# Optimization experiments

Hardware: AMD Instinct MI355X
Metric: run time of the kernel (lower is better)

Reference implementation:

```python
import jax, jax.numpy as jnp
import numpy as np
import math

BATCH, D_MODEL, D_STATE, SEQ_L = 8, 256, 64, 2048


def setup_inputs() -> dict:
    key = jax.random.key(0)
    k0, k1, k2, k3 = jax.random.split(key, 4)
    x = jax.random.normal(k0, (BATCH, D_MODEL, SEQ_L), dtype=jnp.float32)
    # A = -exp(A_real) - 1j*A_imag  (S4D-Lin style init: A = -0.5 + i*pi*n)
    A_real = jnp.full((D_MODEL, D_STATE), jnp.log(0.5), dtype=jnp.float32)
    A_imag = -jnp.broadcast_to(math.pi * jnp.arange(D_STATE, dtype=jnp.float32), (D_MODEL, D_STATE))
    # B, C stored as real view of complex: (1, H, N, 2)
    B = jax.random.normal(k1, (1, D_MODEL, D_STATE, 2), dtype=jnp.float32)
    C = jax.random.normal(k2, (1, D_MODEL, D_STATE, 2), dtype=jnp.float32)
    # inv_dt: log-uniform in [log(1e-3), log(1e-1)], shape (H, 1)
    u = jax.random.uniform(k3, (D_MODEL, 1), dtype=jnp.float32)
    inv_dt = u * (math.log(0.1) - math.log(0.001)) + math.log(0.001)
    return {"x": x, "A_real": A_real, "A_imag": A_imag, "B": B, "C": C, "inv_dt": inv_dt}


def reference(x, A_real, A_imag, B, C, inv_dt):
    L = x.shape[-1]
    # --- _get_params ---
    A = -jnp.exp(A_real) - 1j * A_imag            # (H, N) complex poles
    dt = jnp.exp(inv_dt)                           # (H, 1)
    Bc = B[..., 0] + 1j * B[..., 1]                # (1, H, N)
    Cc = C[..., 0] + 1j * C[..., 1]                # (1, H, N)
    # --- compute_kernel ---
    dtA = dt * A                                   # (H, N) = log of discrete-time pole
    Ceff = (Bc * Cc) * (jnp.exp(dtA) - 1.0) / A    # (1, H, N)
    # log-Vandermonde: K = 2*Re sum_n Ceff * exp(dtA)^l  -> (1, H, L)
    ell = jnp.arange(L, dtype=jnp.float32)
    vand = jnp.exp(dtA[:, :, None] * ell)          # (H, N, L) complex
    k = 2.0 * jnp.real(jnp.einsum('chn,hnl->chl', Ceff, vand))  # (1, H, L)
    # --- FFT convolution ---
    n = 2 * L
    k_f = jnp.fft.rfft(k, n=n)                     # (1, H, L+1)
    x_f = jnp.fft.rfft(x, n=n)                     # (B, H, L+1)
    y_f = jnp.einsum('bhl,chl->bchl', x_f, k_f)    # (B, 1, H, L+1)
    y = jnp.fft.irfft(y_f, n=n)[..., :L]           # (B, 1, H, L)
    return jax.nn.relu(y)
```

## Files before the change

### kernel.cpp

```cpp
#include <hip/hip_runtime.h>


#define B_ 8
#define H_ 256
#define N_ 64
#define L_ 2048
#define Q_ 64
#define NC_ 32
#define COLS_ 128
#define PKSTR_ 68
#define PLSTR_ 72

typedef __attribute__((ext_vector_type(8))) short bf16x8;
typedef __attribute__((ext_vector_type(4))) float f32x4;

#define WS_W1R  0
#define WS_W1I  (WS_W1R + 2097152)
#define WS_TL   (WS_W1I + 2097152)
#define WS_W2R  (WS_TL  + 2097152)
#define WS_W2I  (WS_W2R + 2097152)

#if defined(__has_builtin)
#  if __has_builtin(__builtin_amdgcn_cvt_pk_bf16_f32)
#    define HAVE_CVT_PK 1
#  endif
#endif

__device__ __forceinline__ unsigned short bf16_rne(float f) {
    unsigned int u = __float_as_uint(f);
    u += 0x7FFF + ((u >> 16) & 1);
    return (unsigned short)(u >> 16);
}
__device__ __forceinline__ float bf16_to_f(unsigned short h) {
    return __uint_as_float(((unsigned int)h) << 16);
}
__device__ __forceinline__ unsigned int pack_bf16x2(float a, float b) {
#ifdef HAVE_CVT_PK
    typedef __bf16 bf16v2 __attribute__((ext_vector_type(2)));
    bf16v2 p = __builtin_amdgcn_cvt_pk_bf16_f32(a, b);
    return __builtin_bit_cast(unsigned int, p);
#else
    unsigned int ua = __float_as_uint(a);
    ua += 0x7FFF + ((ua >> 16) & 1);
    unsigned int ub = __float_as_uint(b);
    ub += 0x7FFF + ((ub >> 16) & 1);
    return (ua >> 16) | (ub & 0xFFFF0000u);
#endif
}

__global__ __launch_bounds__(64) void s4d_prep(
    const float* __restrict__ A_real, const float* __restrict__ A_imag,
    const float* __restrict__ Bmat, const float* __restrict__ Cmat,
    const float* __restrict__ inv_dt,
    unsigned short* __restrict__ W1sr, unsigned short* __restrict__ W1si,
    unsigned short* __restrict__ TLs,
    unsigned short* __restrict__ W2sr, unsigned short* __restrict__ W2si)
{
    __shared__ float lds[64 * 68];
    __shared__ float klds[64];

    const int h = blockIdx.x;
    const int n = threadIdx.x;
    const int hn = h * N_ + n;

    const float Ar = -expf(A_real[hn]);
    const float Ai = -A_imag[hn];
    const float dtv = expf(inv_dt[h]);
    const float dr = dtv * Ar;
    const float di = dtv * Ai;
    const float ew = expf(dr);
    float sdi, cdi;
    sincosf(di, &sdi, &cdi);
    const float wr = ew * cdi;
    const float wi = ew * sdi;
    const float em1r = wr - 1.0f;
    const float em1i = wi;
    const float invden = 1.0f / (Ar * Ar + Ai * Ai);
    const float tr = (em1r * Ar + em1i * Ai) * invden;
    const float ti = (em1i * Ar - em1r * Ai) * invden;
    const float br = Bmat[2 * hn], bi = Bmat[2 * hn + 1];
    const float cr = Cmat[2 * hn], ci = Cmat[2 * hn + 1];
    const float bcr = br * cr - bi * ci;
    const float bci = br * ci + bi * cr;
    const float Cr = 2.0f * (bcr * tr - bci * ti);
    const float Ci = 2.0f * (bcr * ti + bci * tr);

    unsigned short* w1r = W1sr + h * 4096;
    unsigned short* w1i = W1si + h * 4096;
    unsigned short* w2r = W2sr + h * 4096;
    unsigned short* w2i = W2si + h * 4096;

    float pr = 1.0f, pi = 0.0f;
    for (int m = 0; m <= 64; ++m) {
        const float qr = Cr * pr - Ci * pi;
        const float qi = Cr * pi + Ci * pr;
        if (m < 64) {
            lds[m * 68 + n] = qr;
            w1r[n * 64 + (63 - m)] = bf16_rne(pr);
            w1i[n * 64 + (63 - m)] = bf16_rne(pi);
        }
        if (m >= 1) {
            w2r[(m - 1) * 64 + n] = bf16_rne(qr);
            w2i[(m - 1) * 64 + n] = bf16_rne(-qi);
        }
        const float npr = pr * wr - pi * wi;
        pi = pr * wi + pi * wr;
        pr = npr;
    }
    __syncthreads();

    float s = 0.0f;
    for (int m = 0; m < 64; ++m) s += lds[n * 68 + m];
    klds[n] = s;
    __syncthreads();

    unsigned short* tl = TLs + h * 4096;
    for (int t = 0; t < 64; ++t) {
        const int d = t - n;
        const float kv = (d >= 0) ? klds[d >= 0 ? d : 0] : 0.0f;
        tl[t * 64 + n] = bf16_rne(kv);
    }
}

__global__ __launch_bounds__(256) void s4d_fused(
    const float* __restrict__ x,
    const float* __restrict__ A_real, const float* __restrict__ A_imag,
    const float* __restrict__ inv_dt,
    const unsigned short* __restrict__ W1sr, const unsigned short* __restrict__ W1si,
    const unsigned short* __restrict__ TLs,
    const unsigned short* __restrict__ W2sr, const unsigned short* __restrict__ W2si,
    float* __restrict__ out)
{
    __shared__ char smem[COLS_ * PLSTR_ * 2 * 2];
    unsigned int*   vpk = (unsigned int*)smem;
    unsigned short* spr = (unsigned short*)smem;
    unsigned short* spi = (unsigned short*)(smem + COLS_ * PLSTR_ * 2);

    const int h     = blockIdx.x >> 1;
    const int bhalf = blockIdx.x & 1;
    const int lane  = threadIdx.x & 63;
    const int wv    = threadIdx.x >> 6;
    const int colw  = wv * 32;
    const int l15   = lane & 15;
    const int quad  = lane >> 4;

    bf16x8 xhi[2][2], xlo[2][2];
    #pragma unroll
    for (int mt = 0; mt < 2; ++mt) {
        const int bc = colw + mt * 16 + l15;
        const int b  = bhalf * 4 + (bc >> 5);
        const int c  = bc & 31;
        const float* xp = x + ((size_t)(b * H_ + h)) * L_ + c * Q_;
        #pragma unroll
        for (int kk = 0; kk < 2; ++kk) {
            const int j0 = kk * 32 + quad * 8;
            const float4 f0 = *(const float4*)(xp + j0);
            const float4 f1 = *(const float4*)(xp + j0 + 4);
            float f[8] = {f0.x, f0.y, f0.z, f0.w, f1.x, f1.y, f1.z, f1.w};
            union { unsigned int u[4]; bf16x8 v; } hi, lo;
            #pragma unroll
            for (int p = 0; p < 4; ++p) {
                const unsigned int hp = pack_bf16x2(f[2 * p], f[2 * p + 1]);
                hi.u[p] = hp;
                const float h0 = __uint_as_float(hp << 16);
                const float h1 = __uint_as_float(hp & 0xFFFF0000u);
                lo.u[p] = pack_bf16x2(f[2 * p] - h0, f[2 * p + 1] - h1);
            }
            xhi[mt][kk] = hi.v;
            xlo[mt][kk] = lo.v;
        }
    }

    float Er, Ei;
    {
        const int hn = h * N_ + lane;
        const float Ar = -expf(A_real[hn]);
        const float Ai = -A_imag[hn];
        const float dtv = expf(inv_dt[h]);
        const float e64 = expf(64.0f * dtv * Ar);
        float s64, c64;
        sincosf(64.0f * dtv * Ai, &s64, &c64);
        Er = e64 * c64;
        Ei = e64 * s64;
    }

    {
        const unsigned short* w1r = W1sr + h * 4096;
        const unsigned short* w1i = W1si + h * 4096;

        f32x4 accr[2][4], acci[2][4];
        #pragma unroll
        for (int a = 0; a < 2; ++a)
            #pragma unroll
            for (int b = 0; b < 4; ++b) { accr[a][b] = (f32x4)0.0f; acci[a][b] = (f32x4)0.0f; }

        #pragma unroll
        for (int nt = 0; nt < 4; ++nt) {
            const int n = nt * 16 + l15;
            bf16x8 brf[2], bif[2];
            #pragma unroll
            for (int kk = 0; kk < 2; ++kk) {
                const int j0 = kk * 32 + quad * 8;
                brf[kk] = *(const bf16x8*)(w1r + n * 64 + j0);
                bif[kk] = *(const bf16x8*)(w1i + n * 64 + j0);
            }
            #pragma unroll
            for (int mt = 0; mt < 2; ++mt)
                #pragma unroll
                for (int kk = 0; kk < 2; ++kk) {
                    accr[mt][nt] = __builtin_amdgcn_mfma_f32_16x16x32_bf16(
                        xhi[mt][kk], brf[kk], accr[mt][nt], 0, 0, 0);
                    acci[mt][nt] = __builtin_amdgcn_mfma_f32_16x16x32_bf16(
                        xhi[mt][kk], bif[kk], acci[mt][nt], 0, 0, 0);
                }
        }

        #pragma unroll
        for (int mt = 0; mt < 2; ++mt)
            #pragma unroll
            for (int nt = 0; nt < 4; ++nt)
                #pragma unroll
                for (int r = 0; r < 4; ++r) {
                    const int bc = colw + mt * 16 + quad * 4 + r;
                    const int n  = nt * 16 + l15;
                    vpk[bc * PKSTR_ + n] =
                        pack_bf16x2(accr[mt][nt][r], acci[mt][nt][r]);
                }
    }
    __syncthreads();

    {
        unsigned int vv[NC_];
        const unsigned int* vp = &vpk[(wv * NC_) * PKSTR_ + lane];
        #pragma unroll
        for (int c = 0; c < NC_; ++c) vv[c] = vp[c * PKSTR_];
        __syncthreads();

        float sr = 0.0f, si = 0.0f;
        unsigned short* pr = &spr[(wv * NC_) * PLSTR_ + lane];
        unsigned short* pi = &spi[(wv * NC_) * PLSTR_ + lane];
        #pragma unroll
        for (int c = 0; c < NC_; ++c) {
            const float vr = __uint_as_float(vv[c] << 16);
            const float vi = __uint_as_float(vv[c] & 0xFFFF0000u);
            const unsigned int sp2 = pack_bf16x2(sr, si);
            pr[c * PLSTR_] = (unsigned short)(sp2 & 0xFFFFu);
            pi[c * PLSTR_] = (unsigned short)(sp2 >> 16);
            const float nsr = fmaf(Er, sr, fmaf(-Ei, si, vr));
            si = fmaf(Ei, sr, fmaf(Er, si, vi));
            sr = nsr;
        }
    }
    __syncthreads();

    {
        const unsigned short* tl  = TLs  + h * 4096;
        const unsigned short* w2r = W2sr + h * 4096;
        const unsigned short* w2i = W2si + h * 4096;

        bf16x8 sr8[2][2], si8[2][2];
        #pragma unroll
        for (int mt = 0; mt < 2; ++mt) {
            const int bc = colw + mt * 16 + l15;
            #pragma unroll
            for (int kk = 0; kk < 2; ++kk) {
                const int j0 = kk * 32 + quad * 8;
                sr8[mt][kk] = *(const bf16x8*)(&spr[bc * PLSTR_ + j0]);
                si8[mt][kk] = *(const bf16x8*)(&spi[bc * PLSTR_ + j0]);
            }
        }

        f32x4 acc[2][4];
        #pragma unroll
        for (int a = 0; a < 2; ++a)
            #pragma unroll
            for (int t = 0; t < 4; ++t) acc[a][t] = (f32x4)0.0f;

        #pragma unroll
        for (int tt = 0; tt < 4; ++tt) {
            const int t = tt * 16 + l15;
            bf16x8 btl[2], bwr[2], bwi[2];
            #pragma unroll
            for (int kk = 0; kk < 2; ++kk) {
                const int j0 = kk * 32 + quad * 8;
                btl[kk] = *(const bf16x8*)(tl  + t * 64 + j0);
                bwr[kk] = *(const bf16x8*)(w2r + t * 64 + j0);
                bwi[kk] = *(const bf16x8*)(w2i + t * 64 + j0);
            }
            #pragma unroll
            for (int mt = 0; mt < 2; ++mt)
                #pragma unroll
                for (int kk = 0; kk < 2; ++kk) {
                    acc[mt][tt] = __builtin_amdgcn_mfma_f32_16x16x32_bf16(
                        xhi[mt][kk], btl[kk], acc[mt][tt], 0, 0, 0);
                    acc[mt][tt] = __builtin_amdgcn_mfma_f32_16x16x32_bf16(
                        xlo[mt][kk], btl[kk], acc[mt][tt], 0, 0, 0);
                    acc[mt][tt] = __builtin_amdgcn_mfma_f32_16x16x32_bf16(
                        sr8[mt][kk], bwr[kk], acc[mt][tt], 0, 0, 0);
                    acc[mt][tt] = __builtin_amdgcn_mfma_f32_16x16x32_bf16(
                        si8[mt][kk], bwi[kk], acc[mt][tt], 0, 0, 0);
                }
        }

        #pragma unroll
        for (int mt = 0; mt < 2; ++mt)
            #pragma unroll
            for (int tt = 0; tt < 4; ++tt)
                #pragma unroll
                for (int r = 0; r < 4; ++r) {
                    const int bc = colw + mt * 16 + quad * 4 + r;
                    const int b  = bhalf * 4 + (bc >> 5);
                    const int c  = bc & 31;
                    const int t  = tt * 16 + l15;
                    out[((size_t)(b * H_ + h)) * L_ + c * Q_ + t] =
                        fmaxf(acc[mt][tt][r], 0.0f);
                }
    }
}

extern "C" void kernel_launch(void* const* d_in, const int* in_sizes, int n_in,
                              void* d_out, int out_size, void* d_ws, size_t ws_size,
                              hipStream_t stream) {
    const float* x      = (const float*)d_in[0];
    const float* A_real = (const float*)d_in[1];
    const float* A_imag = (const float*)d_in[2];
    const float* Bmat   = (const float*)d_in[3];
    const float* Cmat   = (const float*)d_in[4];
    const float* inv_dt = (const float*)d_in[5];
    float* out = (float*)d_out;

    char* ws = (char*)d_ws;
    unsigned short* W1sr = (unsigned short*)(ws + WS_W1R);
    unsigned short* W1si = (unsigned short*)(ws + WS_W1I);
    unsigned short* TLs  = (unsigned short*)(ws + WS_TL);
    unsigned short* W2sr = (unsigned short*)(ws + WS_W2R);
    unsigned short* W2si = (unsigned short*)(ws + WS_W2I);

    s4d_prep<<<dim3(H_), dim3(64), 0, stream>>>(
        A_real, A_imag, Bmat, Cmat, inv_dt, W1sr, W1si, TLs, W2sr, W2si);
    s4d_fused<<<dim3(H_ * 2), dim3(256), 0, stream>>>(
        x, A_real, A_imag, inv_dt, W1sr, W1si, TLs, W2sr, W2si, out);
}
```

Before: 105.5 us.

## Split chunk scan across two waves per batch and double the grid

Each block now handles 2 batches of one head instead of 4. Each wave covers 16 chunks instead of 32, so the grid grows to 1024 blocks and per-thread register use falls. The sequential chunk-state scan is split into two halves: the first-half wave passes its carry through shared memory to the second-half wave, adding a barrier. The goal is more parallelism and occupancy, at the cost of reloading the per-head weights in twice as many blocks and serialising the two scan halves.

```diff
diff --git a/kernel.cpp b/kernel.cpp
--- a/kernel.cpp
+++ b/kernel.cpp
@@ -7,7 +7,7 @@
 #define L_ 2048
 #define Q_ 64
 #define NC_ 32
-#define COLS_ 128
+#define HC_ 16
 #define PKSTR_ 68
 #define PLSTR_ 72
 
@@ -131,26 +131,25 @@
     const unsigned short* __restrict__ W2sr, const unsigned short* __restrict__ W2si,
     float* __restrict__ out)
 {
-    __shared__ char smem[COLS_ * PLSTR_ * 2 * 2];
+    __shared__ char smem[19456];
     unsigned int*   vpk = (unsigned int*)smem;
     unsigned short* spr = (unsigned short*)smem;
-    unsigned short* spi = (unsigned short*)(smem + COLS_ * PLSTR_ * 2);
-
-    const int h     = blockIdx.x >> 1;
-    const int bhalf = blockIdx.x & 1;
-    const int lane  = threadIdx.x & 63;
-    const int wv    = threadIdx.x >> 6;
-    const int colw  = wv * 32;
-    const int l15   = lane & 15;
-    const int quad  = lane >> 4;
-
-    bf16x8 xhi[2][2], xlo[2][2];
-    #pragma unroll
-    for (int mt = 0; mt < 2; ++mt) {
-        const int bc = colw + mt * 16 + l15;
-        const int b  = bhalf * 4 + (bc >> 5);
-        const int c  = bc & 31;
-        const float* xp = x + ((size_t)(b * H_ + h)) * L_ + c * Q_;
+    unsigned short* spi = (unsigned short*)(smem + 9216);
+    float2*         Tx  = (float2*)(smem + 18432);
+
+    const int h    = blockIdx.x & (H_ - 1);
+    const int bp   = blockIdx.x >> 8;
+    const int lane = threadIdx.x & 63;
+    const int wv   = threadIdx.x >> 6;
+    const int b    = bp * 2 + (wv >> 1);
+    const int half = wv & 1;
+    const int l15  = lane & 15;
+    const int quad = lane >> 4;
+    const int rowb = wv * 16;
+
+    bf16x8 xhi[2], xlo[2];
+    {
+        const float* xp = x + ((size_t)(b * H_ + h)) * L_ + (half * HC_ + l15) * Q_;
         #pragma unroll
         for (int kk = 0; kk < 2; ++kk) {
             const int j0 = kk * 32 + quad * 8;
@@ -166,8 +165,8 @@
                 const float h1 = __uint_as_float(hp & 0xFFFF0000u);
                 lo.u[p] = pack_bf16x2(f[2 * p] - h0, f[2 * p + 1] - h1);
             }
-            xhi[mt][kk] = hi.v;
-            xlo[mt][kk] = lo.v;
+            xhi[kk] = hi.v;
+            xlo[kk] = lo.v;
         }
     }
 
@@ -188,67 +187,72 @@
         const unsigned short* w1r = W1sr + h * 4096;
         const unsigned short* w1i = W1si + h * 4096;
 
-        f32x4 accr[2][4], acci[2][4];
-        #pragma unroll
-        for (int a = 0; a < 2; ++a)
-            #pragma unroll
-            for (int b = 0; b < 4; ++b) { accr[a][b] = (f32x4)0.0f; acci[a][b] = (f32x4)0.0f; }
+        f32x4 accr[4], acci[4];
+        #pragma unroll
+        for (int nt = 0; nt < 4; ++nt) { accr[nt] = (f32x4)0.0f; acci[nt] = (f32x4)0.0f; }
 
         #pragma unroll
         for (int nt = 0; nt < 4; ++nt) {
             const int n = nt * 16 + l15;
-            bf16x8 brf[2], bif[2];
             #pragma unroll
             for (int kk = 0; kk < 2; ++kk) {
                 const int j0 = kk * 32 + quad * 8;
-                brf[kk] = *(const bf16x8*)(w1r + n * 64 + j0);
-                bif[kk] = *(const bf16x8*)(w1i + n * 64 + j0);
-            }
-            #pragma unroll
-            for (int mt = 0; mt < 2; ++mt)
-                #pragma unroll
-                for (int kk = 0; kk < 2; ++kk) {
-                    accr[mt][nt] = __builtin_amdgcn_mfma_f32_16x16x32_bf16(
-                        xhi[mt][kk], brf[kk], accr[mt][nt], 0, 0, 0);
-                    acci[mt][nt] = __builtin_amdgcn_mfma_f32_16x16x32_bf16(
-                        xhi[mt][kk], bif[kk], acci[mt][nt], 0, 0, 0);
-                }
-        }
-
-        #pragma unroll
-        for (int mt = 0; mt < 2; ++mt)
-            #pragma unroll
-            for (int nt = 0; nt < 4; ++nt)
-                #pragma unroll
-                for (int r = 0; r < 4; ++r) {
-                    const int bc = colw + mt * 16 + quad * 4 + r;
-                    const int n  = nt * 16 + l15;
-                    vpk[bc * PKSTR_ + n] =
-                        pack_bf16x2(accr[mt][nt][r], acci[mt][nt][r]);
-                }
+                const bf16x8 brf = *(const bf16x8*)(w1r + n * 64 + j0);
+                const bf16x8 bif = *(const bf16x8*)(w1i + n * 64 + j0);
+                accr[nt] = __builtin_amdgcn_mfma_f32_16x16x32_bf16(
+                    xhi[kk], brf, accr[nt], 0, 0, 0);
+                acci[nt] = __builtin_amdgcn_mfma_f32_16x16x32_bf16(
+                    xhi[kk], bif, acci[nt], 0, 0, 0);
+            }
+        }
+
+        #pragma unroll
+        for (int nt = 0; nt < 4; ++nt)
+            #pragma unroll
+            for (int r = 0; r < 4; ++r) {
+                const int row = rowb + quad * 4 + r;
+                const int n   = nt * 16 + l15;
+                vpk[row * PKSTR_ + n] = pack_bf16x2(accr[nt][r], acci[nt][r]);
+            }
     }
     __syncthreads();
 
     {
-        unsigned int vv[NC_];
-        const unsigned int* vp = &vpk[(wv * NC_) * PKSTR_ + lane];
-        #pragma unroll
-        for (int c = 0; c < NC_; ++c) vv[c] = vp[c * PKSTR_];
+        unsigned int vv[HC_];
+        #pragma unroll
+        for (int c = 0; c < HC_; ++c) vv[c] = vpk[(rowb + c) * PKSTR_ + lane];
         __syncthreads();
 
         float sr = 0.0f, si = 0.0f;
-        unsigned short* pr = &spr[(wv * NC_) * PLSTR_ + lane];
-        unsigned short* pi = &spi[(wv * NC_) * PLSTR_ + lane];
-        #pragma unroll
-        for (int c = 0; c < NC_; ++c) {
-            const float vr = __uint_as_float(vv[c] << 16);
-            const float vi = __uint_as_float(vv[c] & 0xFFFF0000u);
-            const unsigned int sp2 = pack_bf16x2(sr, si);
-            pr[c * PLSTR_] = (unsigned short)(sp2 & 0xFFFFu);
-            pi[c * PLSTR_] = (unsigned short)(sp2 >> 16);
-            const float nsr = fmaf(Er, sr, fmaf(-Ei, si, vr));
-            si = fmaf(Ei, sr, fmaf(Er, si, vi));
-            sr = nsr;
+        if (half == 0) {
+            #pragma unroll
+            for (int c = 0; c < HC_; ++c) {
+                const float vr = __uint_as_float(vv[c] << 16);
+                const float vi = __uint_as_float(vv[c] & 0xFFFF0000u);
+                const unsigned int sp2 = pack_bf16x2(sr, si);
+                spr[(rowb + c) * PLSTR_ + lane] = (unsigned short)(sp2 & 0xFFFFu);
+                spi[(rowb + c) * PLSTR_ + lane] = (unsigned short)(sp2 >> 16);
+                const float nsr = fmaf(Er, sr, fmaf(-Ei, si, vr));
+                si = fmaf(Ei, sr, fmaf(Er, si, vi));
+                sr = nsr;
+            }
+            Tx[(wv >> 1) * 64 + lane] = make_float2(sr, si);
+        }
+        __syncthreads();
+        if (half == 1) {
+            const float2 T = Tx[(wv >> 1) * 64 + lane];
+            sr = T.x; si = T.y;
+            #pragma unroll
+            for (int c = 0; c < HC_; ++c) {
+                const float vr = __uint_as_float(vv[c] << 16);
+                const float vi = __uint_as_float(vv[c] & 0xFFFF0000u);
+                const unsigned int sp2 = pack_bf16x2(sr, si);
+                spr[(rowb + c) * PLSTR_ + lane] = (unsigned short)(sp2 & 0xFFFFu);
+                spi[(rowb + c) * PLSTR_ + lane] = (unsigned short)(sp2 >> 16);
+                const float nsr = fmaf(Er, sr, fmaf(-Ei, si, vr));
+                si = fmaf(Ei, sr, fmaf(Er, si, vi));
+                sr = nsr;
+            }
         }
     }
     __syncthreads();
@@ -258,63 +262,47 @@
         const unsigned short* w2r = W2sr + h * 4096;
         const unsigned short* w2i = W2si + h * 4096;
 
-        bf16x8 sr8[2][2], si8[2][2];
-        #pragma unroll
-        for (int mt = 0; mt < 2; ++mt) {
-            const int bc = colw + mt * 16 + l15;
+        bf16x8 sr8[2], si8[2];
+        #pragma unroll
+        for (int kk = 0; kk < 2; ++kk) {
+            const int j0 = kk * 32 + quad * 8;
+            sr8[kk] = *(const bf16x8*)(&spr[(rowb + l15) * PLSTR_ + j0]);
+            si8[kk] = *(const bf16x8*)(&spi[(rowb + l15) * PLSTR_ + j0]);
+        }
+
+        f32x4 acc[4];
+        #pragma unroll
+        for (int tt = 0; tt < 4; ++tt) acc[tt] = (f32x4)0.0f;
+
+        #pragma unroll
+        for (int tt = 0; tt < 4; ++tt) {
+            const int t = tt * 16 + l15;
             #pragma unroll
             for (int kk = 0; kk < 2; ++kk) {
                 const int j0 = kk * 32 + quad * 8;
-                sr8[mt][kk] = *(const bf16x8*)(&spr[bc * PLSTR_ + j0]);
-                si8[mt][kk] = *(const bf16x8*)(&spi[bc * PLSTR_ + j0]);
-            }
-        }
-
-        f32x4 acc[2][4];
-        #pragma unroll
-        for (int a = 0; a < 2; ++a)
-            #pragma unroll
-            for (int t = 0; t < 4; ++t) acc[a][t] = (f32x4)0.0f;
-
-        #pragma unroll
-        for (int tt = 0; tt < 4; ++tt) {
-            const int t = tt * 16 + l15;
-            bf16x8 btl[2], bwr[2], bwi[2];
-            #pragma unroll
-            for (int kk = 0; kk < 2; ++kk) {
-                const int j0 = kk * 32 + quad * 8;
-                btl[kk] = *(const bf16x8*)(tl  + t * 64 + j0);
-                bwr[kk] = *(const bf16x8*)(w2r + t * 64 + j0);
-                bwi[kk] = *(const bf16x8*)(w2i + t * 64 + j0);
-            }
-            #pragma unroll
-            for (int mt = 0; mt < 2; ++mt)
-                #pragma unroll
-                for (int kk = 0; kk < 2; ++kk) {
-                    acc[mt][tt] = __builtin_amdgcn_mfma_f32_16x16x32_bf16(
-                        xhi[mt][kk], btl[kk], acc[mt][tt], 0, 0, 0);
-                    acc[mt][tt] = __builtin_amdgcn_mfma_f32_16x16x32_bf16(
-                        xlo[mt][kk], btl[kk], acc[mt][tt], 0, 0, 0);
-                    acc[mt][tt] = __builtin_amdgcn_mfma_f32_16x16x32_bf16(
-                        sr8[mt][kk], bwr[kk], acc[mt][tt], 0, 0, 0);
-                    acc[mt][tt] = __builtin_amdgcn_mfma_f32_16x16x32_bf16(
-                        si8[mt][kk], bwi[kk], acc[mt][tt], 0, 0, 0);
-                }
-        }
-
-        #pragma unroll
-        for (int mt = 0; mt < 2; ++mt)
-            #pragma unroll
-            for (int tt = 0; tt < 4; ++tt)
-                #pragma unroll
-                for (int r = 0; r < 4; ++r) {
-                    const int bc = colw + mt * 16 + quad * 4 + r;
-                    const int b  = bhalf * 4 + (bc >> 5);
-                    const int c  = bc & 31;
-                    const int t  = tt * 16 + l15;
-                    out[((size_t)(b * H_ + h)) * L_ + c * Q_ + t] =
-                        fmaxf(acc[mt][tt][r], 0.0f);
-                }
+                const bf16x8 btl = *(const bf16x8*)(tl  + t * 64 + j0);
+                const bf16x8 bwr = *(const bf16x8*)(w2r + t * 64 + j0);
+                const bf16x8 bwi = *(const bf16x8*)(w2i + t * 64 + j0);
+                acc[tt] = __builtin_amdgcn_mfma_f32_16x16x32_bf16(
+                    xhi[kk], btl, acc[tt], 0, 0, 0);
+                acc[tt] = __builtin_amdgcn_mfma_f32_16x16x32_bf16(
+                    xlo[kk], btl, acc[tt], 0, 0, 0);
+                acc[tt] = __builtin_amdgcn_mfma_f32_16x16x32_bf16(
+                    sr8[kk], bwr, acc[tt], 0, 0, 0);
+                acc[tt] = __builtin_amdgcn_mfma_f32_16x16x32_bf16(
+                    si8[kk], bwi, acc[tt], 0, 0, 0);
+            }
+        }
+
+        #pragma unroll
+        for (int tt = 0; tt < 4; ++tt)
+            #pragma unroll
+            for (int r = 0; r < 4; ++r) {
+                const int c = half * HC_ + quad * 4 + r;
+                const int t = tt * 16 + l15;
+                out[((size_t)(b * H_ + h)) * L_ + c * Q_ + t] =
+                    fmaxf(acc[tt][r], 0.0f);
+            }
     }
 }
 
@@ -338,6 +326,6 @@
 
     s4d_prep<<<dim3(H_), dim3(64), 0, stream>>>(
         A_real, A_imag, Bmat, Cmat, inv_dt, W1sr, W1si, TLs, W2sr, W2si);
-    s4d_fused<<<dim3(H_ * 2), dim3(256), 0, stream>>>(
+    s4d_fused<<<dim3(H_ * 4), dim3(256), 0, stream>>>(
         x, A_real, A_imag, inv_dt, W1sr, W1si, TLs, W2sr, W2si, out);
 }
```

Result: slower. 116.9 us (+10.9%).

## Parallelize prep kernel over 4x threads with vectorized stores and precomputed E

Applied to the files above, without the earlier changes.

The prep kernel now uses 256 threads per head. Each thread computes a 16- or 17-step segment of the power sequence, seeding it directly with exp/sincos, instead of one thread walking all 64 steps serially. W1, TL and W2 are written as 16-byte vector stores through LDS staging instead of scattered 2-byte stores. The per-pole E = w^64 is computed once in prep and read by the fused kernel rather than recomputed with exp/sincos. This shortens the serial prep critical path and improves write coalescing, at the cost of more LDS and slightly different rounding from the segment seeds.

```diff
diff --git a/kernel.cpp b/kernel.cpp
--- a/kernel.cpp
+++ b/kernel.cpp
@@ -19,6 +19,7 @@
 #define WS_TL   (WS_W1I + 2097152)
 #define WS_W2R  (WS_TL  + 2097152)
 #define WS_W2I  (WS_W2R + 2097152)
+#define WS_E    (WS_W2I + 2097152)
 
 #if defined(__has_builtin)
 #  if __has_builtin(__builtin_amdgcn_cvt_pk_bf16_f32)
@@ -48,20 +49,24 @@
 #endif
 }
 
-__global__ __launch_bounds__(64) void s4d_prep(
+__global__ __launch_bounds__(256) void s4d_prep(
     const float* __restrict__ A_real, const float* __restrict__ A_imag,
     const float* __restrict__ Bmat, const float* __restrict__ Cmat,
     const float* __restrict__ inv_dt,
     unsigned short* __restrict__ W1sr, unsigned short* __restrict__ W1si,
     unsigned short* __restrict__ TLs,
-    unsigned short* __restrict__ W2sr, unsigned short* __restrict__ W2si)
+    unsigned short* __restrict__ W2sr, unsigned short* __restrict__ W2si,
+    float2* __restrict__ Earr)
 {
-    __shared__ float lds[64 * 68];
+    __shared__ float qr_l[65 * 66];
+    __shared__ float qi_l[65 * 66];
     __shared__ float klds[64];
 
-    const int h = blockIdx.x;
-    const int n = threadIdx.x;
-    const int hn = h * N_ + n;
+    const int h   = blockIdx.x;
+    const int tid = threadIdx.x;
+    const int n   = tid >> 2;
+    const int blk = tid & 3;
+    const int hn  = h * N_ + n;
 
     const float Ar = -expf(A_real[hn]);
     const float Ai = -A_imag[hn];
@@ -85,47 +90,88 @@
     const float Cr = 2.0f * (bcr * tr - bci * ti);
     const float Ci = 2.0f * (bcr * ti + bci * tr);
 
-    unsigned short* w1r = W1sr + h * 4096;
-    unsigned short* w1i = W1si + h * 4096;
-    unsigned short* w2r = W2sr + h * 4096;
-    unsigned short* w2i = W2si + h * 4096;
-
-    float pr = 1.0f, pi = 0.0f;
-    for (int m = 0; m <= 64; ++m) {
-        const float qr = Cr * pr - Ci * pi;
-        const float qi = Cr * pi + Ci * pr;
-        if (m < 64) {
-            lds[m * 68 + n] = qr;
-            w1r[n * 64 + (63 - m)] = bf16_rne(pr);
-            w1i[n * 64 + (63 - m)] = bf16_rne(pi);
-        }
-        if (m >= 1) {
-            w2r[(m - 1) * 64 + n] = bf16_rne(qr);
-            w2i[(m - 1) * 64 + n] = bf16_rne(-qi);
-        }
-        const float npr = pr * wr - pi * wi;
-        pi = pr * wi + pi * wr;
-        pr = npr;
+    {
+        const int m0 = 48 - 16 * blk;
+        const float e0 = expf((float)m0 * dr);
+        float s0, c0;
+        sincosf((float)m0 * di, &s0, &c0);
+        float pr = e0 * c0, pi = e0 * s0;
+        union { unsigned short u16[16]; uint4 q[2]; } tr_, ti_;
+        #pragma unroll
+        for (int i = 0; i < 16; ++i) {
+            tr_.u16[15 - i] = bf16_rne(pr);
+            ti_.u16[15 - i] = bf16_rne(pi);
+            const float npr = pr * wr - pi * wi;
+            pi = pr * wi + pi * wr;
+            pr = npr;
+        }
+        uint4* d0 = (uint4*)(W1sr + (size_t)h * 4096 + n * 64 + blk * 16);
+        d0[0] = tr_.q[0]; d0[1] = tr_.q[1];
+        uint4* d1 = (uint4*)(W1si + (size_t)h * 4096 + n * 64 + blk * 16);
+        d1[0] = ti_.q[0]; d1[1] = ti_.q[1];
+    }
+
+    {
+        const int m0   = blk * 17;
+        const int mcnt = (blk == 3) ? 14 : 17;
+        const float e0 = expf((float)m0 * dr);
+        float s0, c0;
+        sincosf((float)m0 * di, &s0, &c0);
+        float pr = e0 * c0, pi = e0 * s0;
+        for (int i = 0; i < mcnt; ++i) {
+            const int m = m0 + i;
+            qr_l[m * 66 + n] = Cr * pr - Ci * pi;
+            qi_l[m * 66 + n] = Cr * pi + Ci * pr;
+            const float npr = pr * wr - pi * wi;
+            pi = pr * wi + pi * wr;
+            pr = npr;
+        }
     }
     __syncthreads();
 
-    float s = 0.0f;
-    for (int m = 0; m < 64; ++m) s += lds[n * 68 + m];
-    klds[n] = s;
+    if (tid < 64) {
+        float s = 0.0f;
+        for (int j = 0; j < 64; ++j) s += qr_l[tid * 66 + j];
+        klds[tid] = s;
+
+        const int hn2 = h * N_ + tid;
+        const float Ar2 = -expf(A_real[hn2]);
+        const float Ai2 = -A_imag[hn2];
+        const float e64 = expf(64.0f * dtv * Ar2);
+        float s64, c64;
+        sincosf(64.0f * dtv * (-Ai2) * -1.0f, &s64, &c64);
+        Earr[hn2] = make_float2(e64 * c64, e64 * s64);
+    }
     __syncthreads();
 
-    unsigned short* tl = TLs + h * 4096;
-    for (int t = 0; t < 64; ++t) {
-        const int d = t - n;
-        const float kv = (d >= 0) ? klds[d >= 0 ? d : 0] : 0.0f;
-        tl[t * 64 + n] = bf16_rne(kv);
+    {
+        const int t = tid >> 2;
+        union { unsigned short u16[16]; uint4 q[2]; } a_, b_;
+        #pragma unroll
+        for (int i = 0; i < 16; ++i) {
+            const int j = blk * 16 + i;
+            const int d = t - j;
+            a_.u16[i] = bf16_rne(d >= 0 ? klds[d >= 0 ? d : 0] : 0.0f);
+        }
+        uint4* dtl = (uint4*)(TLs + (size_t)h * 4096 + t * 64 + blk * 16);
+        dtl[0] = a_.q[0]; dtl[1] = a_.q[1];
+
+        #pragma unroll
+        for (int i = 0; i < 16; ++i) {
+            const int nn = blk * 16 + i;
+            a_.u16[i] = bf16_rne(qr_l[(t + 1) * 66 + nn]);
+            b_.u16[i] = bf16_rne(-qi_l[(t + 1) * 66 + nn]);
+        }
+        uint4* d2r = (uint4*)(W2sr + (size_t)h * 4096 + t * 64 + blk * 16);
+        d2r[0] = a_.q[0]; d2r[1] = a_.q[1];
+        uint4* d2i = (uint4*)(W2si + (size_t)h * 4096 + t * 64 + blk * 16);
+        d2i[0] = b_.q[0]; d2i[1] = b_.q[1];
     }
 }
 
 __global__ __launch_bounds__(256) void s4d_fused(
     const float* __restrict__ x,
-    const float* __restrict__ A_real, const float* __restrict__ A_imag,
-    const float* __restrict__ inv_dt,
+    const float2* __restrict__ Earr,
     const unsigned short* __restrict__ W1sr, const unsigned short* __restrict__ W1si,
     const unsigned short* __restrict__ TLs,
     const unsigned short* __restrict__ W2sr, const unsigned short* __restrict__ W2si,
@@ -171,18 +217,8 @@
         }
     }
 
-    float Er, Ei;
-    {
-        const int hn = h * N_ + lane;
-        const float Ar = -expf(A_real[hn]);
-        const float Ai = -A_imag[hn];
-        const float dtv = expf(inv_dt[h]);
-        const float e64 = expf(64.0f * dtv * Ar);
-        float s64, c64;
-        sincosf(64.0f * dtv * Ai, &s64, &c64);
-        Er = e64 * c64;
-        Ei = e64 * s64;
-    }
+    const float2 E = Earr[h * N_ + lane];
+    const float Er = E.x, Ei = E.y;
 
     {
         const unsigned short* w1r = W1sr + h * 4096;
@@ -335,9 +371,10 @@
     unsigned short* TLs  = (unsigned short*)(ws + WS_TL);
     unsigned short* W2sr = (unsigned short*)(ws + WS_W2R);
     unsigned short* W2si = (unsigned short*)(ws + WS_W2I);
-
-    s4d_prep<<<dim3(H_), dim3(64), 0, stream>>>(
-        A_real, A_imag, Bmat, Cmat, inv_dt, W1sr, W1si, TLs, W2sr, W2si);
+    float2*         Earr = (float2*)(ws + WS_E);
+
+    s4d_prep<<<dim3(H_), dim3(256), 0, stream>>>(
+        A_real, A_imag, Bmat, Cmat, inv_dt, W1sr, W1si, TLs, W2sr, W2si, Earr);
     s4d_fused<<<dim3(H_ * 2), dim3(256), 0, stream>>>(
-        x, A_real, A_imag, inv_dt, W1sr, W1si, TLs, W2sr, W2si, out);
-}
+        x, Earr, W1sr, W1si, TLs, W2sr, W2si, out);
+}
```

After: 96.32 us. 8.7% less time.
